# Performance work log

Measured on AMD Instinct MI355X. Metric: run time of the kernel, lower is better.

## Reference

```python
import jax, jax.numpy as jnp
from jax import lax
import numpy as np

B = 256
EMB_DIM = 64
N_EMB = 512
LAT1 = 1024   # 16 slots * 64
LAT2 = 512
LAT = LAT1 + LAT2  # 1536
COMMIT = 0.25
EMB_COST = 1.0


def setup_inputs() -> dict:
    key = jax.random.key(0)
    ks = iter(jax.random.split(key, 40))

    def w(shape, fan_in):
        return jax.random.normal(next(ks), shape, jnp.float32) * np.float32(1.0 / np.sqrt(fan_in))

    def b(n):
        return jax.random.normal(next(ks), (n,), jnp.float32) * np.float32(0.01)

    inp = {}
    inp['x'] = jax.random.normal(next(ks), (B, 3, 64, 64), jnp.float32)
    # encoder convs, torch OIHW layout, k=4
    inp['ew0'] = w((64, 3, 4, 4), 3 * 16);   inp['eb0'] = b(64)
    inp['ew1'] = w((64, 64, 4, 4), 64 * 16); inp['eb1'] = b(64)
    inp['ew2'] = w((128, 64, 4, 4), 64 * 16); inp['eb2'] = b(128)
    inp['ew3'] = w((256, 128, 4, 4), 128 * 16); inp['eb3'] = b(256)
    # encoder fc11: 4096 -> 1024 -> 1024 -> 1536, stored (in,out)
    inp['fw0'] = w((4096, 1024), 4096); inp['fb0'] = b(1024)
    inp['fw1'] = w((1024, 1024), 1024); inp['fb1'] = b(1024)
    inp['fw2'] = w((1024, LAT), 1024);  inp['fb2'] = b(LAT)
    # VQ codebook
    inp['codebook'] = jax.random.normal(next(ks), (N_EMB, EMB_DIM), jnp.float32)
    # decoder fc3: 1536 -> 512 -> 1024 -> 4096
    inp['gw0'] = w((LAT, 512), LAT);    inp['gb0'] = b(512)
    inp['gw1'] = w((512, 1024), 512);   inp['gb1'] = b(1024)
    inp['gw2'] = w((1024, 4096), 1024); inp['gb2'] = b(4096)
    # decoder ConvTranspose2d weights, torch layout (Cin, Cout, kh, kw)
    inp['tw0'] = w((256, 128, 4, 4), 256 * 16); inp['tb0'] = b(128)
    inp['tw1'] = w((128, 64, 4, 4), 128 * 16);  inp['tb1'] = b(64)
    inp['tw2'] = w((64, 64, 4, 4), 64 * 16);    inp['tb2'] = b(64)
    inp['tw3'] = w((64, 3, 4, 4), 64 * 16);     inp['tb3'] = b(3)
    return inp


def _conv(x, w, b):
    # Conv2d k=4 s=2 p=1 -> halves H,W
    y = lax.conv_general_dilated(x, w, (2, 2), ((1, 1), (1, 1)),
                                 dimension_numbers=('NCHW', 'OIHW', 'NCHW'))
    return y + b[None, :, None, None]


def _convt(x, w, b):
    # ConvTranspose2d k=4 s=2 p=1 -> doubles H,W.
    # Equivalent to lhs_dilation=2, pad k-1-p=2, flipped kernel, swapped I/O.
    wf = jnp.flip(w, (2, 3)).transpose(1, 0, 2, 3)
    y = lax.conv_general_dilated(x, wf, (1, 1), ((2, 2), (2, 2)),
                                 lhs_dilation=(2, 2),
                                 dimension_numbers=('NCHW', 'OIHW', 'NCHW'))
    return y + b[None, :, None, None]


def _forward(x, ew0, eb0, ew1, eb1, ew2, eb2, ew3, eb3,
             fw0, fb0, fw1, fb1, fw2, fb2, codebook,
             gw0, gb0, gw1, gb1, gw2, gb2,
             tw0, tb0, tw1, tb1, tw2, tb2, tw3, tb3):
    relu = jax.nn.relu
    # --- encoder conv stack (last conv has no ReLU) ---
    h = relu(_conv(x, ew0, eb0))
    h = relu(_conv(h, ew1, eb1))
    h = relu(_conv(h, ew2, eb2))
    h = _conv(h, ew3, eb3)                      # [B,256,4,4]
    h = h.reshape(h.shape[0], -1)               # [B,4096]
    h = relu(h @ fw0 + fb0)
    h = relu(h @ fw1 + fb1)
    z = h @ fw2 + fb2                           # [B,1536]
    # --- split content / style (isVQStyle=False) ---
    z_c = z[:, :LAT1]
    z_s = z[:, LAT1:]
    # --- vector quantize z_c (16 slots of dim 64, shared codebook) ---
    flat = z_c.reshape(-1, EMB_DIM)             # [B*16, 64]
    d = (jnp.sum(flat * flat, axis=1, keepdims=True)
         + jnp.sum(codebook * codebook, axis=1)
         - 2.0 * flat @ codebook.T)             # [B*16, 512]
    idx = jnp.argmin(d, axis=1)
    quantized = codebook[idx].reshape(z_c.shape)  # [B,1024]
    sg = lax.stop_gradient
    q_latent_loss = jnp.mean((quantized - sg(z_c)) ** 2) * EMB_COST
    e_latent_loss = jnp.mean((z_c - sg(quantized)) ** 2) * COMMIT
    loss = q_latent_loss + e_latent_loss
    quantized = z_c + sg(quantized - z_c)       # straight-through
    e = jnp.concatenate([quantized, z_s], axis=-1)  # [B,1536]
    # --- decoder ---
    g = relu(e @ gw0 + gb0)
    g = relu(g @ gw1 + gb1)
    g = (g @ gw2 + gb2).reshape(-1, 256, 4, 4)
    g = relu(_convt(g, tw0, tb0))
    g = relu(_convt(g, tw1, tb1))
    g = relu(_convt(g, tw2, tb2))
    x_recon = _convt(g, tw3, tb3)               # [B,3,64,64]
    return x_recon, loss


def reference(x, ew0, eb0, ew1, eb1, ew2, eb2, ew3, eb3,
              fw0, fb0, fw1, fb1, fw2, fb2, codebook,
              gw0, gb0, gw1, gb1, gw2, gb2,
              tw0, tb0, tw1, tb1, tw2, tb2, tw3, tb3):
    return _forward(x, ew0, eb0, ew1, eb1, ew2, eb2, ew3, eb3,
                    fw0, fb0, fw1, fb1, fw2, fb2, codebook,
                    gw0, gb0, gw1, gb1, gw2, gb2,
                    tw0, tb0, tw1, tb1, tw2, tb2, tw3, tb3)
```

## Files before the change

### kernel.cpp

```cpp
#include <hip/hip_runtime.h>
#include <hip/hip_bf16.h>


#define TPB 256
typedef __attribute__((ext_vector_type(8))) short short8v;
typedef __attribute__((ext_vector_type(4))) float f32x4;
typedef unsigned int u32;
typedef unsigned short u16;

__device__ inline u16 f2bf(float x){
  union { __hip_bfloat16 b; u16 u; } cv;
  cv.b = __float2bfloat16(x);
  return cv.u;
}
__device__ inline float bf2f(u16 h){ union{u32 u;float f;}v; v.u=((u32)h)<<16; return v.f;}
__device__ inline u32 packhl(float x){ u16 h=f2bf(x); u16 l=f2bf(x-bf2f(h)); return ((u32)l<<16)|(u32)h;}

template<int NS>
__device__ inline void splitN(float x, u16 t[3]) {
  u16 h0 = f2bf(x); t[0] = h0;
  float r1 = x - bf2f(h0);
  u16 h1 = f2bf(r1); t[1] = h1;
  if (NS == 3) { float r2 = r1 - bf2f(h1); t[2] = f2bf(r2); }
}

template<int NS, int ST>
__device__ inline void stW(u32* L, int row, int oct, const u16 hs[3][8]) {
  constexpr int SWM = (ST == 64) ? 15 : 7;
  const int sw = row & SWM;
#pragma unroll
  for (int s = 0; s < NS; ++s) {
    uint4 d;
    d.x = (u32)hs[s][0] | ((u32)hs[s][1] << 16);
    d.y = (u32)hs[s][2] | ((u32)hs[s][3] << 16);
    d.z = (u32)hs[s][4] | ((u32)hs[s][5] << 16);
    d.w = (u32)hs[s][6] | ((u32)hs[s][7] << 16);
    int ch = (((s << 2) | oct) ^ sw) << 2;
    *reinterpret_cast<uint4*>(&L[row * ST + ch]) = d;
  }
}

template<int NS, int ST>
__device__ inline void stWf(u32* L, int row, int oct, const float v[8]) {
  u16 hs[3][8];
#pragma unroll
  for (int e = 0; e < 8; ++e) {
    u16 t3[3]; splitN<NS>(v[e], t3);
    hs[0][e] = t3[0]; hs[1][e] = t3[1]; if (NS == 3) hs[2][e] = t3[2];
  }
  stW<NS, ST>(L, row, oct, hs);
}

template<int ST>
__device__ inline void stWp(u32* L, int row, int oct, int s, uint4 d) {
  constexpr int SWM = (ST == 64) ? 15 : 7;
  int ch = (((s << 2) | oct) ^ (row & SWM)) << 2;
  *reinterpret_cast<uint4*>(&L[row * ST + ch]) = d;
}

template<int ST>
__device__ inline short8v rdFrag(const u32* L, int row, int c) {
  constexpr int SWM = (ST == 64) ? 15 : 7;
  int ph = (c ^ (row & SWM)) << 2;
  return *reinterpret_cast<const short8v*>(&L[row * ST + ph]);
}

__global__ __launch_bounds__(TPB) void wsplit3_k(
    const float* __restrict__ src, u16* __restrict__ dst, int n)
{
  for (int i = blockIdx.x * TPB + threadIdx.x; i < n; i += gridDim.x * TPB) {
    u16 t3[3]; splitN<3>(src[i], t3);
    dst[i] = t3[0]; dst[i + n] = t3[1]; dst[i + 2 * n] = t3[2];
  }
}
__global__ __launch_bounds__(TPB) void wprep2_k(
    const float* __restrict__ src, u16* __restrict__ dh, u16* __restrict__ dl,
    int Ci, int Co)
{
  int K4 = Ci << 2;
  int tot = 4 * Co * K4;
  for (int i = blockIdx.x * TPB + threadIdx.x; i < tot; i += gridDim.x * TPB) {
    int par = i / (Co * K4); int rem = i - par * (Co * K4);
    int co = rem / K4; int k4 = rem - co * K4;
    int ci = k4 >> 2, ay = (k4 >> 1) & 1, ax = k4 & 1;
    int py = par >> 1, px = par & 1;
    int widx = ((1 - py) << 2) + (1 - px) + (ay << 3) + (ax << 1);
    float x = src[(((size_t)ci * Co + co) << 4) + widx];
    u16 h = f2bf(x);
    dh[i] = h; dl[i] = f2bf(x - bf2f(h));
  }
}

__global__ __launch_bounds__(TPB) void x_pad_k(
    const float* __restrict__ x, float* __restrict__ xp)
{
  int idx = blockIdx.x * TPB + threadIdx.x;
  if (idx >= 3345408) return;
  int px = idx % 66; int t = idx / 66; int py = t % 66; int p = t / 66;
  float v = 0.f;
  if (py >= 1 && py <= 64 && px >= 1 && px <= 64)
    v = x[(size_t)p * 4096 + (py - 1) * 64 + (px - 1)];
  xp[idx] = v;
}
__global__ __launch_bounds__(TPB) void zb0_k(float* __restrict__ h0p)
{
  int idx = blockIdx.x * TPB + threadIdx.x;
  if (idx >= 2162688) return;
  int p = idx / 132, k = idx % 132;
  int py, px;
  if (k < 34)       { py = 0;           px = k; }
  else if (k < 68)  { py = 33;          px = k - 34; }
  else if (k < 100) { py = k - 68 + 1;  px = 0; }
  else              { py = k - 100 + 1; px = 33; }
  h0p[(size_t)p * 1156 + py * 34 + px] = 0.f;
}

template<int RM, int OUTM>
__global__ __launch_bounds__(TPB, 2) void conv_ad(
    const float* __restrict__ in, const u16* __restrict__ wsp,
    const float* __restrict__ bias, float* __restrict__ outp,
    int Ci, int Co, int Wi, int lwo, int relu, int KSPL, int PS,
    int bS, int ciS, int Mtot)
{
  constexpr int BM = RM * 64;
  __shared__ __align__(16) u32 BL[2][64 * 64];
  const int K = Ci << 4;
  const int PW = Wi + 2;
  const int Wo = Wi >> 1;
  const int tid = threadIdx.x;
  const int m0 = blockIdx.x * BM, n0 = blockIdx.y << 6;
  const int lane = tid & 63, wv = tid >> 6, r = lane & 15, g = lane >> 4;
  const int kb0 = blockIdx.z * KSPL;
  const int kbN = min(kb0 + KSPL, K);
  const int khsel = g & 1;
  const int cig = g >> 1;
  f32x4 acc[RM][4] = {};

  int base[RM];
#pragma unroll
  for (int mm = 0; mm < RM; ++mm) {
    int cell = m0 + (wv * RM + mm) * 16 + r;
    int x = cell & (Wo - 1), y = (cell >> lwo) & (Wo - 1), b = cell >> (lwo + lwo);
    base[mm] = b * bS + (2 * y + 2 * khsel) * PW + 2 * x;
  }

  auto gA = [&](int kb, float v[RM][8]) {
    if ((kb + (g << 3)) < K) {
      int cioff = ((kb >> 4) + cig) * ciS;
#pragma unroll
      for (int mm = 0; mm < RM; ++mm) {
        const float* p = in + base[mm] + cioff;
#pragma unroll
        for (int e = 0; e < 8; ++e)
          v[mm][e] = p[(e >> 2) * PW + (e & 3)];
      }
    } else {
#pragma unroll
      for (int mm = 0; mm < RM; ++mm)
#pragma unroll
        for (int e = 0; e < 8; ++e) v[mm][e] = 0.f;
    }
  };
  auto gB = [&](int kb, uint4* d) {
    int n = tid & 63, oc2 = tid >> 6;
    int k8 = kb + (oc2 << 3);
    if (k8 < K) {
      const u16* wp = wsp + (size_t)(n0 + n) * K + k8;
      d[0] = *reinterpret_cast<const uint4*>(wp);
      d[1] = *reinterpret_cast<const uint4*>(wp + PS);
      d[2] = *reinterpret_cast<const uint4*>(wp + 2 * PS);
    } else {
      d[0] = d[1] = d[2] = make_uint4(0u, 0u, 0u, 0u);
    }
  };
  auto mkfrags = [&](const float v[8], short8v f[3]) {
    u16 hs[3][8];
#pragma unroll
    for (int e = 0; e < 8; ++e) {
      u16 t3[3]; splitN<3>(v[e], t3);
      hs[0][e] = t3[0]; hs[1][e] = t3[1]; hs[2][e] = t3[2];
    }
#pragma unroll
    for (int s = 0; s < 3; ++s) {
      union { u16 u[8]; short8v sv; } cv;
#pragma unroll
      for (int e = 0; e < 8; ++e) cv.u[e] = hs[s][e];
      f[s] = cv.sv;
    }
  };

  float vA[RM][8], vA2[RM][8];
  uint4 vB[3], vB2[3];
  gA(kb0, vA); gB(kb0, vB);
  for (int kb = kb0; kb < kbN; kb += 32) {
    u32* BLc = BL[((kb - kb0) >> 5) & 1];
    {
      int n = tid & 63, oc2 = tid >> 6;
      stWp<64>(BLc, n, oc2, 0, vB[0]);
      stWp<64>(BLc, n, oc2, 1, vB[1]);
      stWp<64>(BLc, n, oc2, 2, vB[2]);
    }
    const bool more = (kb + 32) < kbN;
    if (more) { gB(kb + 32, vB2); gA(kb + 32, vA2); }
    short8v a_[RM][3];
#pragma unroll
    for (int mm = 0; mm < RM; ++mm) mkfrags(vA[mm], a_[mm]);
    __syncthreads();
#pragma unroll
    for (int ns = 0; ns < 4; ++ns) {
      short8v b_[3];
#pragma unroll
      for (int s = 0; s < 3; ++s) b_[s] = rdFrag<64>(BLc, (ns << 4) + r, (s << 2) | g);
#pragma unroll
      for (int mm = 0; mm < RM; ++mm) {
        acc[mm][ns] = __builtin_amdgcn_mfma_f32_16x16x32_bf16(a_[mm][0], b_[0], acc[mm][ns], 0, 0, 0);
        acc[mm][ns] = __builtin_amdgcn_mfma_f32_16x16x32_bf16(a_[mm][0], b_[1], acc[mm][ns], 0, 0, 0);
        acc[mm][ns] = __builtin_amdgcn_mfma_f32_16x16x32_bf16(a_[mm][1], b_[0], acc[mm][ns], 0, 0, 0);
        acc[mm][ns] = __builtin_amdgcn_mfma_f32_16x16x32_bf16(a_[mm][1], b_[1], acc[mm][ns], 0, 0, 0);
        acc[mm][ns] = __builtin_amdgcn_mfma_f32_16x16x32_bf16(a_[mm][0], b_[2], acc[mm][ns], 0, 0, 0);
        acc[mm][ns] = __builtin_amdgcn_mfma_f32_16x16x32_bf16(a_[mm][2], b_[0], acc[mm][ns], 0, 0, 0);
      }
    }
    if (more) {
#pragma unroll
      for (int mm = 0; mm < RM; ++mm)
#pragma unroll
        for (int e = 0; e < 8; ++e) vA[mm][e] = vA2[mm][e];
#pragma unroll
      for (int s = 0; s < 3; ++s) vB[s] = vB2[s];
    }
  }
#pragma unroll
  for (int mm = 0; mm < RM; ++mm)
#pragma unroll
    for (int ns = 0; ns < 4; ++ns) {
      int c0 = m0 + (wv * RM + mm) * 16 + (g << 2);
      int co = n0 + (ns << 4) + r;
      if (OUTM == 0) {
        float bv = bias[co];
        const int OPW = Wo + 2;
        const int OPHW = OPW * OPW;
#pragma unroll
        for (int q = 0; q < 4; ++q) {
          int cell = c0 + q;
          int x = cell & (Wo - 1), y = (cell >> lwo) & (Wo - 1), b = cell >> (lwo + lwo);
          float v = acc[mm][ns][q] + bv;
          if (relu) v = fmaxf(v, 0.f);
          outp[((size_t)(b * Co + co)) * OPHW + (y + 1) * OPW + (x + 1)] = v;
        }
      } else {
        float4 o;
        o.x = acc[mm][ns][0]; o.y = acc[mm][ns][1];
        o.z = acc[mm][ns][2]; o.w = acc[mm][ns][3];
        *reinterpret_cast<float4*>(
            &outp[((size_t)(blockIdx.z * Co + co)) * Mtot + c0]) = o;
      }
    }
}

__global__ __launch_bounds__(TPB) void combine_cm_k(
    const float* __restrict__ P, const float* __restrict__ bias,
    float* __restrict__ out)
{
  int idx = blockIdx.x * TPB + threadIdx.x;
  if (idx >= 5308416) return;
  int px = idx % 18; int t = idx / 18; int py = t % 18; t /= 18;
  int b = t % 256; int co = t / 256;
  float v = 0.f;
  if (py >= 1 && py <= 16 && px >= 1 && px <= 16) {
    int cell = b * 256 + (py - 1) * 16 + (px - 1);
    v = P[(size_t)co * 65536 + cell] + P[(size_t)(64 + co) * 65536 + cell] + bias[co];
    v = fmaxf(v, 0.f);
  }
  out[idx] = v;
}

__global__ __launch_bounds__(TPB) void combine_pad_k(
    const float* __restrict__ P, const float* __restrict__ bias,
    float* __restrict__ out)
{
  int idx = blockIdx.x * TPB + threadIdx.x;
  if (idx >= 3276800) return;
  int px = idx % 10; int t = idx / 10; int py = t % 10; t /= 10;
  int co = t % 128; int b = t / 128;
  float v = 0.f;
  if (py >= 1 && py <= 8 && px >= 1 && px <= 8) {
    int cell = b * 64 + (py - 1) * 8 + (px - 1);
    float s = 0.f;
#pragma unroll
    for (int z = 0; z < 4; ++z)
      s += P[((size_t)(z * 128 + co)) * 16384 + cell];
    v = fmaxf(s + bias[co], 0.f);
  }
  out[idx] = v;
}

__global__ __launch_bounds__(TPB) void conv_combine(
    const float* __restrict__ P, const float* __restrict__ bias,
    float* __restrict__ out, int Mtot, int N, int SK, int lwo, int relu)
{
  int idx = blockIdx.x * TPB + threadIdx.x;
  int mq = Mtot >> 2;
  int co = idx / mq;
  int cell0 = (idx - co * mq) << 2;
  if (co >= N) return;
  float4 s = make_float4(0.f, 0.f, 0.f, 0.f);
  for (int z = 0; z < SK; ++z) {
    const float4 pv = *reinterpret_cast<const float4*>(
        &P[((size_t)z * N + co) * Mtot + cell0]);
    s.x += pv.x; s.y += pv.y; s.z += pv.z; s.w += pv.w;
  }
  float bv = bias[co];
  s.x += bv; s.y += bv; s.z += bv; s.w += bv;
  if (relu) { s.x = fmaxf(s.x, 0.f); s.y = fmaxf(s.y, 0.f);
              s.z = fmaxf(s.z, 0.f); s.w = fmaxf(s.w, 0.f); }
  int Wo = 1 << lwo;
  int x = cell0 & (Wo - 1), y = (cell0 >> lwo) & (Wo - 1), b = cell0 >> (lwo + lwo);
  *reinterpret_cast<float4*>(&out[(((size_t)b * N + co) * Wo + y) * Wo + x]) = s;
}

template<int NS, int OUTM>
__global__ __launch_bounds__(TPB) void gemm_mf(
    const float* __restrict__ A, const float* __restrict__ W,
    const float* __restrict__ bias, void* __restrict__ outp,
    int M, int K, int N, int KSPL)
{
  constexpr int ST = (NS == 3) ? 64 : 32;
  __shared__ __align__(16) u32 L[(64 + 64) * ST];
  u32* AL = L; u32* BL = L + 64 * ST;
  const int tid = threadIdx.x;
  const int m0 = blockIdx.x << 6, n0 = blockIdx.y << 6;
  const int lane = tid & 63, wv = tid >> 6, r = lane & 15, g = lane >> 4;
  const int kb0 = blockIdx.z * KSPL;
  const int kbN = kb0 + KSPL;
  const int cl = tid & 63, oct = tid >> 6;
  f32x4 acc[4] = {};

  float vA[8], vB[8], vA2[8], vB2[8];
  auto gA = [&](int kt, float* v) {
    const float* ap = &A[(size_t)(m0 + cl) * K + kt + (oct << 3)];
    *reinterpret_cast<float4*>(&v[0]) = *reinterpret_cast<const float4*>(ap);
    *reinterpret_cast<float4*>(&v[4]) = *reinterpret_cast<const float4*>(ap + 4);
  };
  auto gB = [&](int kt, float* v) {
#pragma unroll
    for (int e = 0; e < 8; ++e)
      v[e] = W[(size_t)(kt + (oct << 3) + e) * N + n0 + cl];
  };

  gA(kb0, vA); gB(kb0, vB);
  for (int kt = kb0; kt < kbN; kt += 32) {
    const bool more = (kt + 32) < kbN;
    if (more) { gA(kt + 32, vA2); gB(kt + 32, vB2); }
    stWf<NS, ST>(AL, cl, oct, vA);
    stWf<NS, ST>(BL, cl, oct, vB);
    __syncthreads();
    short8v a_[3];
#pragma unroll
    for (int s = 0; s < NS; ++s) a_[s] = rdFrag<ST>(AL, (wv << 4) + r, (s << 2) | g);
#pragma unroll
    for (int ns = 0; ns < 4; ++ns) {
      short8v b_[3];
#pragma unroll
      for (int s = 0; s < NS; ++s) b_[s] = rdFrag<ST>(BL, (ns << 4) + r, (s << 2) | g);
      acc[ns] = __builtin_amdgcn_mfma_f32_16x16x32_bf16(a_[0], b_[0], acc[ns], 0, 0, 0);
      acc[ns] = __builtin_amdgcn_mfma_f32_16x16x32_bf16(a_[0], b_[1], acc[ns], 0, 0, 0);
      acc[ns] = __builtin_amdgcn_mfma_f32_16x16x32_bf16(a_[1], b_[0], acc[ns], 0, 0, 0);
      if (NS == 3) {
        acc[ns] = __builtin_amdgcn_mfma_f32_16x16x32_bf16(a_[1], b_[1], acc[ns], 0, 0, 0);
        acc[ns] = __builtin_amdgcn_mfma_f32_16x16x32_bf16(a_[0], b_[2], acc[ns], 0, 0, 0);
        acc[ns] = __builtin_amdgcn_mfma_f32_16x16x32_bf16(a_[2], b_[0], acc[ns], 0, 0, 0);
      }
    }
    __syncthreads();
    if (more) {
#pragma unroll
      for (int e = 0; e < 8; ++e) { vA[e] = vA2[e]; vB[e] = vB2[e]; }
    }
  }
#pragma unroll
  for (int ns = 0; ns < 4; ++ns)
#pragma unroll
    for (int q = 0; q < 4; ++q) {
      int m = m0 + (wv << 4) + (g << 2) + q;
      int n = n0 + (ns << 4) + r;
      float v = acc[ns][q];
      if (OUTM == 0) ((float*)outp)[((size_t)blockIdx.z * M + m) * N + n] = v;
      else           ((u32*)outp)[(size_t)m * N + n] = packhl(v + bias[n]);
    }
}

__global__ __launch_bounds__(TPB) void combine_k(
    const float* __restrict__ P, const float* __restrict__ bias,
    float* __restrict__ out, int MN, int N, int SK, int relu)
{
  int i4 = (blockIdx.x * TPB + threadIdx.x) << 2;
  if (i4 >= MN) return;
  float4 s = make_float4(0.f, 0.f, 0.f, 0.f);
  for (int z = 0; z < SK; ++z) {
    const float4 pv = *reinterpret_cast<const float4*>(&P[(size_t)z * MN + i4]);
    s.x += pv.x; s.y += pv.y; s.z += pv.z; s.w += pv.w;
  }
  int n = i4 % N;
  s.x += bias[n]; s.y += bias[n + 1]; s.z += bias[n + 2]; s.w += bias[n + 3];
  if (relu) { s.x = fmaxf(s.x, 0.f); s.y = fmaxf(s.y, 0.f);
              s.z = fmaxf(s.z, 0.f); s.w = fmaxf(s.w, 0.f); }
  *reinterpret_cast<float4*>(&out[i4]) = s;
}

__global__ __launch_bounds__(TPB) void combine_pk_k(
    const float* __restrict__ P, const float* __restrict__ bias,
    u32* __restrict__ out)
{
  int i4 = (blockIdx.x * TPB + threadIdx.x) << 2;
  if (i4 >= 1048576) return;
  const float4 p0 = *reinterpret_cast<const float4*>(&P[i4]);
  const float4 p1 = *reinterpret_cast<const float4*>(&P[1048576 + i4]);
  int n = i4 % 4096;
  uint4 o;
  o.x = packhl(p0.x + p1.x + bias[n]);
  o.y = packhl(p0.y + p1.y + bias[n + 1]);
  o.z = packhl(p0.z + p1.z + bias[n + 2]);
  o.w = packhl(p0.w + p1.w + bias[n + 3]);
  *reinterpret_cast<uint4*>(&out[i4]) = o;
}

template<int RM, int EMIT, int SPLITIN>
__global__ __launch_bounds__(TPB) void convt_ad(
    const u32* __restrict__ in, const u16* __restrict__ wth,
    const u16* __restrict__ wtl, const float* __restrict__ bias,
    u32* __restrict__ outq, int Ci, int Co, int Hi, int lwi, int relu)
{
  constexpr int BM = RM * 64;
  constexpr int STC = BM + 4;
  constexpr int LB = 2 * 64 * 32;
  constexpr int LSZ = (LB > 16 * STC) ? LB : 16 * STC;
  __shared__ __align__(16) u32 L[LSZ];
  const int Wi = Hi, K4 = Ci << 2;
  const int HW = Hi * Wi, HWq = HW >> 2, Wiq = Wi >> 1;
  const int par = blockIdx.z, py = par >> 1, px = par & 1;
  const int tid = threadIdx.x;
  const int m0 = blockIdx.x * BM, n0 = blockIdx.y << 6;
  const int lane = tid & 63, wv = tid >> 6, r = lane & 15, g = lane >> 4;
  const int stepCi = SPLITIN ? HWq : HW;
  f32x4 acc[RM][4] = {};

  int offT[RM][4]; u32 mskT[RM][4];
#pragma unroll
  for (int mm = 0; mm < RM; ++mm) {
    int cell = m0 + (wv * RM + mm) * 16 + r;
    int X = cell & (Wi - 1), Y = (cell >> lwi) & (Wi - 1), b = cell >> (lwi + lwi);
#pragma unroll
    for (int t = 0; t < 4; ++t) {
      int ay = t >> 1, ax = t & 1;
      int gy = Y + py - ay, gx = X + px - ax;
      bool ok = (gy >= 0 && gy < Hi && gx >= 0 && gx < Wi);
      int gyc = min(max(gy, 0), Hi - 1), gxc = min(max(gx, 0), Wi - 1);
      if (SPLITIN) {
        int q = ((gyc & 1) << 1) | (gxc & 1);
        offT[mm][t] = q * (256 * Ci * HWq) + b * Ci * HWq + (gyc >> 1) * Wiq + (gxc >> 1);
      } else {
        offT[mm][t] = b * Ci * HW + gyc * Wi + gxc;
      }
      mskT[mm][t] = ok ? 0xffffffffu : 0u;
    }
  }

  auto gB = [&](int kb, uint4* d) {
    int n = tid & 63, oc2 = tid >> 6;
    size_t base = (size_t)(par * Co + n0 + n) * K4 + kb + (oc2 << 3);
    d[0] = *reinterpret_cast<const uint4*>(wth + base);
    d[1] = *reinterpret_cast<const uint4*>(wtl + base);
  };

  uint4 vB[2], vB2[2];
  gB(0, vB);
  u32 vA[RM][8];
  int cur = 0;
  for (int kb = 0; kb < K4; kb += 32) {
    {
      int cib = ((kb >> 2) + (g << 1)) * stepCi;
#pragma unroll
      for (int mm = 0; mm < RM; ++mm)
#pragma unroll
        for (int e = 0; e < 8; ++e) {
          int t = e & 3;
          vA[mm][e] = in[offT[mm][t] + cib + ((e >> 2) ? stepCi : 0)] & mskT[mm][t];
        }
    }
    u32* BLc = L + cur * (64 * 32);
    {
      int n = tid & 63, oc2 = tid >> 6;
      stWp<32>(BLc, n, oc2, 0, vB[0]);
      stWp<32>(BLc, n, oc2, 1, vB[1]);
    }
    const bool more = (kb + 32) < K4;
    if (more) gB(kb + 32, vB2);
    __syncthreads();
    short8v a_[RM][2];
#pragma unroll
    for (int mm = 0; mm < RM; ++mm) {
      const u32* v = vA[mm];
      union { uint4 u; short8v s; } ch, clo;
      ch.u.x = (v[0] & 0xffffu) | (v[1] << 16);  clo.u.x = (v[0] >> 16) | (v[1] & 0xffff0000u);
      ch.u.y = (v[2] & 0xffffu) | (v[3] << 16);  clo.u.y = (v[2] >> 16) | (v[3] & 0xffff0000u);
      ch.u.z = (v[4] & 0xffffu) | (v[5] << 16);  clo.u.z = (v[4] >> 16) | (v[5] & 0xffff0000u);
      ch.u.w = (v[6] & 0xffffu) | (v[7] << 16);  clo.u.w = (v[6] >> 16) | (v[7] & 0xffff0000u);
      a_[mm][0] = ch.s; a_[mm][1] = clo.s;
    }
#pragma unroll
    for (int ns = 0; ns < 4; ++ns) {
      short8v b_[2];
#pragma unroll
      for (int s = 0; s < 2; ++s) b_[s] = rdFrag<32>(BLc, (ns << 4) + r, (s << 2) | g);
#pragma unroll
      for (int mm = 0; mm < RM; ++mm) {
        acc[mm][ns] = __builtin_amdgcn_mfma_f32_16x16x32_bf16(a_[mm][0], b_[0], acc[mm][ns], 0, 0, 0);
        acc[mm][ns] = __builtin_amdgcn_mfma_f32_16x16x32_bf16(a_[mm][0], b_[1], acc[mm][ns], 0, 0, 0);
        acc[mm][ns] = __builtin_amdgcn_mfma_f32_16x16x32_bf16(a_[mm][1], b_[0], acc[mm][ns], 0, 0, 0);
      }
    }
    if (more) { vB[0] = vB2[0]; vB[1] = vB2[1]; }
    cur ^= 1;
  }
  const size_t QO = (size_t)256 * Co * HW;
  u32* op = outq + (size_t)par * QO;
  constexpr int C4N = BM / 4;
#pragma unroll
  for (int ph = 0; ph < 4; ++ph) {
    __syncthreads();
    float bv = bias[n0 + (ph << 4) + r];
#pragma unroll
    for (int mm = 0; mm < RM; ++mm)
#pragma unroll
      for (int q = 0; q < 4; ++q) {
        int cell = (wv * RM + mm) * 16 + (g << 2) + q;
        float v = acc[mm][ph][q] + bv;
        if (relu) v = fmaxf(v, 0.f);
        L[r * STC + cell] = EMIT ? packhl(v) : __float_as_uint(v);
      }
    __syncthreads();
#pragma unroll
    for (int it = 0; it < RM; ++it) {
      int lin = it * TPB + tid;
      int c4 = lin & (C4N - 1);
      int colL = lin / C4N;
      int col = (ph << 4) + colL;
      int cell0 = c4 << 2;
      uint4 d = *reinterpret_cast<const uint4*>(&L[colL * STC + cell0]);
      int gc = m0 + cell0;
      int Xo = gc & (Wi - 1), Yo = (gc >> lwi) & (Wi - 1), bo = gc >> (lwi + lwi);
      *reinterpret_cast<uint4*>(
          &op[((size_t)(bo * Co + n0 + col) * Hi + Yo) * Wi + Xo]) = d;
    }
  }
}

__global__ __launch_bounds__(TPB) void convt3_kernel(
    const float* __restrict__ inq, const float* __restrict__ w,
    float* __restrict__ part)
{
  __shared__ float wl[3072];
  __shared__ float il[8][33 * 32];
  const int b = blockIdx.x;
  const int z = blockIdx.y;
  const int tid = threadIdx.x;
  for (int i = tid; i < 3072; i += TPB) wl[i] = w[i];
  const int Y = tid >> 3;
  const int X0 = (tid & 7) << 2;
  float acc[3][2][8];
#pragma unroll
  for (int o = 0; o < 3; ++o)
#pragma unroll
    for (int p = 0; p < 2; ++p)
#pragma unroll
      for (int q = 0; q < 8; ++q) acc[o][p][q] = 0.f;

  const int cbeg = z << 5, cend = cbeg + 32;
  for (int c0 = cbeg; c0 < cend; c0 += 8) {
    __syncthreads();
    for (int i = tid; i < 8192; i += TPB) {
      int cc = i >> 10, yy = (i >> 5) & 31, xx = i & 31;
      int q = ((yy & 1) << 1) | (xx & 1);
      il[cc][yy * 33 + xx] = inq[(size_t)q * 4194304 +
          (((size_t)b * 64 + c0 + cc) * 16 + (yy >> 1)) * 16 + (xx >> 1)];
    }
    __syncthreads();
    for (int cc = 0; cc < 8; ++cc) {
      float iv[3][6];
#pragma unroll
      for (int j = 0; j < 3; ++j) {
        int gy = Y - 1 + j;
        int gyc = min(max(gy, 0), 31);
        float my = (gy >= 0 && gy < 32) ? 1.f : 0.f;
#pragma unroll
        for (int k = 0; k < 6; ++k) {
          int gx = X0 - 1 + k;
          int gxc = min(max(gx, 0), 31);
          float mx = (gx >= 0 && gx < 32) ? 1.f : 0.f;
          iv[j][k] = il[cc][gyc * 33 + gxc] * (my * mx);
        }
      }
      const float* wq = &wl[(c0 + cc) * 48];
#pragma unroll
      for (int o = 0; o < 3; ++o) {
        const float* wo = wq + o * 16;
#pragma unroll
        for (int c = 0; c < 4; ++c) {
          acc[o][0][2*c]   = fmaf(iv[1][c+1], wo[5],  acc[o][0][2*c]);
          acc[o][0][2*c]   = fmaf(iv[1][c],   wo[7],  acc[o][0][2*c]);
          acc[o][0][2*c]   = fmaf(iv[0][c+1], wo[13], acc[o][0][2*c]);
          acc[o][0][2*c]   = fmaf(iv[0][c],   wo[15], acc[o][0][2*c]);
          acc[o][0][2*c+1] = fmaf(iv[1][c+2], wo[4],  acc[o][0][2*c+1]);
          acc[o][0][2*c+1] = fmaf(iv[1][c+1], wo[6],  acc[o][0][2*c+1]);
          acc[o][0][2*c+1] = fmaf(iv[0][c+2], wo[12], acc[o][0][2*c+1]);
          acc[o][0][2*c+1] = fmaf(iv[0][c+1], wo[14], acc[o][0][2*c+1]);
          acc[o][1][2*c]   = fmaf(iv[2][c+1], wo[1],  acc[o][1][2*c]);
          acc[o][1][2*c]   = fmaf(iv[2][c],   wo[3],  acc[o][1][2*c]);
          acc[o][1][2*c]   = fmaf(iv[1][c+1], wo[9],  acc[o][1][2*c]);
          acc[o][1][2*c]   = fmaf(iv[1][c],   wo[11], acc[o][1][2*c]);
          acc[o][1][2*c+1] = fmaf(iv[2][c+2], wo[0],  acc[o][1][2*c+1]);
          acc[o][1][2*c+1] = fmaf(iv[2][c+1], wo[2],  acc[o][1][2*c+1]);
          acc[o][1][2*c+1] = fmaf(iv[1][c+2], wo[8],  acc[o][1][2*c+1]);
          acc[o][1][2*c+1] = fmaf(iv[1][c+1], wo[10], acc[o][1][2*c+1]);
        }
      }
    }
  }
  float* pz = part + (size_t)z * 3145728;
#pragma unroll
  for (int o = 0; o < 3; ++o) {
#pragma unroll
    for (int p = 0; p < 2; ++p) {
      float* op = pz + (((size_t)b * 3 + o) * 64 + 2 * Y + p) * 64 + 2 * X0;
      *reinterpret_cast<float4*>(op) =
          make_float4(acc[o][p][0], acc[o][p][1], acc[o][p][2], acc[o][p][3]);
      *reinterpret_cast<float4*>(op + 4) =
          make_float4(acc[o][p][4], acc[o][p][5], acc[o][p][6], acc[o][p][7]);
    }
  }
}

__global__ __launch_bounds__(TPB) void c3_combine(
    const float* __restrict__ part, const float* __restrict__ bias,
    float* __restrict__ out)
{
  int i4 = (blockIdx.x * TPB + threadIdx.x) << 2;
  const float4 p0 = *reinterpret_cast<const float4*>(&part[i4]);
  const float4 p1 = *reinterpret_cast<const float4*>(&part[i4 + 3145728]);
  int o = (i4 >> 12) % 3;
  float bv = bias[o];
  float4 s = make_float4(p0.x + p1.x + bv, p0.y + p1.y + bv,
                         p0.z + p1.z + bv, p0.w + p1.w + bv);
  *reinterpret_cast<float4*>(&out[i4]) = s;
}

__global__ __launch_bounds__(TPB) void vq8_kernel(
    const float* __restrict__ z, const float* __restrict__ cb,
    float* __restrict__ e, float* __restrict__ rowloss)
{
  __shared__ float cbL[64][65];
  __shared__ float zr[8][64];
  const int tid = threadIdx.x;
  const int lane = tid & 63, wid = tid >> 6;
  const int r0 = blockIdx.x << 3;

  for (int i = tid; i < 512; i += TPB) {
    int rr = i >> 6, k = i & 63;
    int row = r0 + rr;
    int b = row >> 4, s = row & 15;
    zr[rr][k] = z[(size_t)b * 1536 + s * 64 + k];
  }

  float best[2] = {3.4e38f, 3.4e38f};
  int bi[2] = {0, 0};

  for (int c0 = 0; c0 < 512; c0 += 64) {
    __syncthreads();
#pragma unroll
    for (int i = 0; i < 4; ++i) {
      int j = (tid >> 4) + (i << 4);
      int kq = tid & 15;
      const float4 v = *reinterpret_cast<const float4*>(
          &cb[(size_t)(c0 + j) * 64 + (kq << 2)]);
      cbL[(kq << 2) + 0][j] = v.x;
      cbL[(kq << 2) + 1][j] = v.y;
      cbL[(kq << 2) + 2][j] = v.z;
      cbL[(kq << 2) + 3][j] = v.w;
    }
    __syncthreads();
#pragma unroll
    for (int rep = 0; rep < 2; ++rep) {
      const float* zp = zr[wid + (rep << 2)];
      float d = 0.f;
#pragma unroll
      for (int k = 0; k < 64; ++k) {
        float t = zp[k] - cbL[k][lane];
        d = fmaf(t, t, d);
      }
      if (d < best[rep]) { best[rep] = d; bi[rep] = c0 + lane; }
    }
  }
#pragma unroll
  for (int rep = 0; rep < 2; ++rep) {
#pragma unroll
    for (int off = 32; off > 0; off >>= 1) {
      float ob = __shfl_xor(best[rep], off);
      int   oi = __shfl_xor(bi[rep], off);
      if (ob < best[rep] || (ob == best[rep] && oi < bi[rep])) {
        best[rep] = ob; bi[rep] = oi;
      }
    }
    int row = r0 + wid + (rep << 2);
    int b = row >> 4, s = row & 15;
    e[(size_t)b * 1536 + s * 64 + lane] = cb[(size_t)bi[rep] * 64 + lane];
    if (lane == 0) rowloss[row] = best[rep];
  }
}

__global__ __launch_bounds__(TPB) void zs_copy_kernel(
    const float* __restrict__ z, float* __restrict__ e)
{
  int i = blockIdx.x * TPB + threadIdx.x;
  int b = i >> 9, k = i & 511;
  e[(size_t)b * 1536 + 1024 + k] = z[(size_t)b * 1536 + 1024 + k];
}

__global__ __launch_bounds__(TPB) void loss_reduce_kernel(
    const float* __restrict__ rl, float* __restrict__ out)
{
  __shared__ float sm[TPB];
  float s = 0.f;
  for (int i = threadIdx.x; i < 4096; i += TPB) s += rl[i];
  sm[threadIdx.x] = s;
  __syncthreads();
  for (int sft = 128; sft > 0; sft >>= 1) {
    if (threadIdx.x < sft) sm[threadIdx.x] += sm[threadIdx.x + sft];
    __syncthreads();
  }
  if (threadIdx.x == 0) out[0] = sm[0] * (1.25f / 262144.f);
}

extern "C" void kernel_launch(void* const* d_in, const int* in_sizes, int n_in,
                              void* d_out, int out_size, void* d_ws, size_t ws_size,
                              hipStream_t stream)
{
  const float* x    = (const float*)d_in[0];
  const float* ew0  = (const float*)d_in[1];
  const float* eb0  = (const float*)d_in[2];
  const float* ew1  = (const float*)d_in[3];
  const float* eb1  = (const float*)d_in[4];
  const float* ew2  = (const float*)d_in[5];
  const float* eb2  = (const float*)d_in[6];
  const float* ew3  = (const float*)d_in[7];
  const float* eb3  = (const float*)d_in[8];
  const float* fw0  = (const float*)d_in[9];
  const float* fb0  = (const float*)d_in[10];
  const float* fw1  = (const float*)d_in[11];
  const float* fb1  = (const float*)d_in[12];
  const float* fw2  = (const float*)d_in[13];
  const float* fb2  = (const float*)d_in[14];
  const float* cb   = (const float*)d_in[15];
  const float* gw0  = (const float*)d_in[16];
  const float* gb0  = (const float*)d_in[17];
  const float* gw1  = (const float*)d_in[18];
  const float* gb1  = (const float*)d_in[19];
  const float* gw2  = (const float*)d_in[20];
  const float* gb2  = (const float*)d_in[21];
  const float* tw0  = (const float*)d_in[22];
  const float* tb0  = (const float*)d_in[23];
  const float* tw1  = (const float*)d_in[24];
  const float* tb1  = (const float*)d_in[25];
  const float* tw2  = (const float*)d_in[26];
  const float* tb2  = (const float*)d_in[27];
  const float* tw3  = (const float*)d_in[28];
  const float* tb3  = (const float*)d_in[29];

  float* out = (float*)d_out;
  float* ws  = (float*)d_ws;

  u16*   WE0  = (u16*)(ws + 0);
  u16*   WE1  = (u16*)(ws + 4608);
  u16*   WE2  = (u16*)(ws + 102912);
  u16*   WE3  = (u16*)(ws + 299520);
  float* RL   = ws + 1085952;
  float* H0P  = ws + 1090048;
  float* PC1  = ws + 20029952;
  float* XP   = ws + 20029952;
  float* H1P  = ws + 1090048;
  float* PC23 = ws + 6398464;
  float* H2P  = ws + 14787072;
  float* H3   = ws + 18063872;
  float* P    = ws + 1090048;
  float* F0   = ws + 5284352;
  float* F1   = ws + 5546496;
  float* Z    = ws + 5808640;
  float* E    = ws + 6201856;
  float* G0   = ws + 6595072;
  float* G1   = ws + 6726144;
  float* T2S  = ws + 1090048;
  u16*   WT0h = (u16*)(ws + 17867264);
  u16*   WT0l = (u16*)(ws + 18129408);
  u16*   WT1h = (u16*)(ws + 18391552);
  u16*   WT1l = (u16*)(ws + 18457088);
  u16*   WT2h = (u16*)(ws + 18522624);
  u16*   WT2l = (u16*)(ws + 18555392);
  float* PG2  = ws + 18588160;
  u32*   G2P  = (u32*)(ws + 20685312);
  u32*   T0S  = (u32*)(ws + 21733888);
  u32*   T1S  = (u32*)(ws + 23831040);
  float* PT3  = ws + 18588160;

  wsplit3_k<<<dim3(12),  TPB, 0, stream>>>(ew0, WE0, 3072);
  wsplit3_k<<<dim3(256), TPB, 0, stream>>>(ew1, WE1, 65536);
  wsplit3_k<<<dim3(512), TPB, 0, stream>>>(ew2, WE2, 131072);
  wsplit3_k<<<dim3(1024),TPB, 0, stream>>>(ew3, WE3, 524288);
  x_pad_k<<<dim3(13068), TPB, 0, stream>>>(x, XP);
  zb0_k<<<dim3(8448), TPB, 0, stream>>>(H0P);

  conv_ad<4,0><<<dim3(1024, 1, 1), TPB, 0, stream>>>(
      XP, WE0, eb0, H0P, 3, 64, 64, 5, 1, 48, 3072, 13068, 4356, 0);
  conv_ad<4,1><<<dim3(256, 1, 2), TPB, 0, stream>>>(
      H0P, WE1, eb1, PC1, 64, 64, 32, 4, 1, 512, 65536, 73984, 1156, 65536);
  combine_cm_k<<<dim3(20736), TPB, 0, stream>>>(PC1, eb1, H1P);
  conv_ad<4,1><<<dim3(64, 2, 4), TPB, 0, stream>>>(
      H1P, WE2, eb2, PC23, 64, 128, 16, 3, 1, 256, 131072, 324, 82944, 16384);
  combine_pad_k<<<dim3(12800), TPB, 0, stream>>>(PC23, eb2, H2P);
  conv_ad<4,1><<<dim3(16, 4, 8), TPB, 0, stream>>>(
      H2P, WE3, eb3, PC23, 128, 256, 8, 2, 0, 256, 524288, 12800, 100, 4096);
  conv_combine<<<dim3(1024), TPB, 0, stream>>>(PC23, eb3, H3, 4096, 256, 8, 2, 0);

  gemm_mf<3,0><<<dim3(4, 16, 16), TPB, 0, stream>>>(H3, fw0, fb0, (void*)P, 256, 4096, 1024, 256);
  combine_k<<<dim3(256), TPB, 0, stream>>>(P, fb0, F0, 262144, 1024, 16, 1);
  gemm_mf<3,0><<<dim3(4, 16, 8), TPB, 0, stream>>>(F0, fw1, fb1, (void*)P, 256, 1024, 1024, 128);
  combine_k<<<dim3(256), TPB, 0, stream>>>(P, fb1, F1, 262144, 1024, 8, 1);
  gemm_mf<3,0><<<dim3(4, 24, 8), TPB, 0, stream>>>(F1, fw2, fb2, (void*)P, 256, 1024, 1536, 128);
  combine_k<<<dim3(384), TPB, 0, stream>>>(P, fb2, Z, 393216, 1536, 8, 0);

  vq8_kernel<<<dim3(512), TPB, 0, stream>>>(Z, cb, E, RL);
  zs_copy_kernel<<<dim3(512), TPB, 0, stream>>>(Z, E);
  loss_reduce_kernel<<<dim3(1), TPB, 0, stream>>>(RL, out + (size_t)out_size - 1);

  gemm_mf<2,0><<<dim3(4, 8, 8), TPB, 0, stream>>>(E,  gw0, gb0, (void*)P, 256, 1536, 512, 192);
  combine_k<<<dim3(128), TPB, 0, stream>>>(P, gb0, G0, 131072, 512, 8, 1);
  gemm_mf<2,0><<<dim3(4, 16, 4), TPB, 0, stream>>>(G0, gw1, gb1, (void*)P, 256, 512, 1024, 128);
  combine_k<<<dim3(256), TPB, 0, stream>>>(P, gb1, G1, 262144, 1024, 4, 1);

  wprep2_k<<<dim3(512), TPB, 0, stream>>>(tw0, WT0h, WT0l, 256, 128);
  wprep2_k<<<dim3(128), TPB, 0, stream>>>(tw1, WT1h, WT1l, 128, 64);
  wprep2_k<<<dim3(64),  TPB, 0, stream>>>(tw2, WT2h, WT2l, 64, 64);

  gemm_mf<2,0><<<dim3(4, 64, 2), TPB, 0, stream>>>(G1, gw2, gb2, (void*)PG2, 256, 1024, 4096, 512);
  combine_pk_k<<<dim3(1024), TPB, 0, stream>>>(PG2, gb2, G2P);

  convt_ad<2,1,0><<<dim3(32, 2, 4),  TPB, 0, stream>>>(G2P, WT0h, WT0l, tb0, T0S, 256, 128, 4,  2, 1);
  convt_ad<4,1,1><<<dim3(64, 1, 4),  TPB, 0, stream>>>(T0S, WT1h, WT1l, tb1, T1S, 128, 64,  8,  3, 1);
  convt_ad<4,0,1><<<dim3(256, 1, 4), TPB, 0, stream>>>(T1S, WT2h, WT2l, tb2, (u32*)T2S, 64, 64, 16, 4, 1);
  convt3_kernel<<<dim3(256, 2), TPB, 0, stream>>>(T2S, tw3, PT3);
  c3_combine<<<dim3(3072), TPB, 0, stream>>>(PT3, tb3, out);
}
```

Measured before the change: 536.1 us.

## Drop split-bf16 precision in decoder GEMM and transposed convs to single bf16

Switches the last decoder FC and the three transposed-conv layers from a hi/lo bf16 split (three MFMAs per product) to plain single bf16 (one MFMA). Weight prep now emits only the high half, and activations are packed as a single bf16. The convt kernel also prefetches the A operand into registers one step ahead and uses smaller row tiles with more blocks. This removes most MFMA work and halves the weight traffic in these layers, at the cost of reduced accuracy that may exceed the tolerance.

Result: faster. 508.8 us (-5.1%).

```diff
diff --git a/kernel.cpp b/kernel.cpp
--- a/kernel.cpp
+++ b/kernel.cpp
@@ -14,7 +14,6 @@
   return cv.u;
 }
 __device__ inline float bf2f(u16 h){ union{u32 u;float f;}v; v.u=((u32)h)<<16; return v.f;}
-__device__ inline u32 packhl(float x){ u16 h=f2bf(x); u16 l=f2bf(x-bf2f(h)); return ((u32)l<<16)|(u32)h;}
 
 template<int NS>
 __device__ inline void splitN(float x, u16 t[3]) {
@@ -45,7 +44,7 @@
   u16 hs[3][8];
 #pragma unroll
   for (int e = 0; e < 8; ++e) {
-    u16 t3[3]; splitN<NS>(v[e], t3);
+    u16 t3[3]; splitN<(NS == 3) ? 3 : 2>(v[e], t3);
     hs[0][e] = t3[0]; hs[1][e] = t3[1]; if (NS == 3) hs[2][e] = t3[2];
   }
   stW<NS, ST>(L, row, oct, hs);
@@ -73,9 +72,8 @@
     dst[i] = t3[0]; dst[i + n] = t3[1]; dst[i + 2 * n] = t3[2];
   }
 }
-__global__ __launch_bounds__(TPB) void wprep2_k(
-    const float* __restrict__ src, u16* __restrict__ dh, u16* __restrict__ dl,
-    int Ci, int Co)
+__global__ __launch_bounds__(TPB) void wprep1_k(
+    const float* __restrict__ src, u16* __restrict__ dh, int Ci, int Co)
 {
   int K4 = Ci << 2;
   int tot = 4 * Co * K4;
@@ -85,9 +83,7 @@
     int ci = k4 >> 2, ay = (k4 >> 1) & 1, ax = k4 & 1;
     int py = par >> 1, px = par & 1;
     int widx = ((1 - py) << 2) + (1 - px) + (ay << 3) + (ax << 1);
-    float x = src[(((size_t)ci * Co + co) << 4) + widx];
-    u16 h = f2bf(x);
-    dh[i] = h; dl[i] = f2bf(x - bf2f(h));
+    dh[i] = f2bf(src[(((size_t)ci * Co + co) << 4) + widx]);
   }
 }
 
@@ -364,8 +360,10 @@
 #pragma unroll
       for (int s = 0; s < NS; ++s) b_[s] = rdFrag<ST>(BL, (ns << 4) + r, (s << 2) | g);
       acc[ns] = __builtin_amdgcn_mfma_f32_16x16x32_bf16(a_[0], b_[0], acc[ns], 0, 0, 0);
-      acc[ns] = __builtin_amdgcn_mfma_f32_16x16x32_bf16(a_[0], b_[1], acc[ns], 0, 0, 0);
-      acc[ns] = __builtin_amdgcn_mfma_f32_16x16x32_bf16(a_[1], b_[0], acc[ns], 0, 0, 0);
+      if (NS >= 2) {
+        acc[ns] = __builtin_amdgcn_mfma_f32_16x16x32_bf16(a_[0], b_[1], acc[ns], 0, 0, 0);
+        acc[ns] = __builtin_amdgcn_mfma_f32_16x16x32_bf16(a_[1], b_[0], acc[ns], 0, 0, 0);
+      }
       if (NS == 3) {
         acc[ns] = __builtin_amdgcn_mfma_f32_16x16x32_bf16(a_[1], b_[1], acc[ns], 0, 0, 0);
         acc[ns] = __builtin_amdgcn_mfma_f32_16x16x32_bf16(a_[0], b_[2], acc[ns], 0, 0, 0);
@@ -386,7 +384,7 @@
       int n = n0 + (ns << 4) + r;
       float v = acc[ns][q];
       if (OUTM == 0) ((float*)outp)[((size_t)blockIdx.z * M + m) * N + n] = v;
-      else           ((u32*)outp)[(size_t)m * N + n] = packhl(v + bias[n]);
+      else           ((u32*)outp)[(size_t)m * N + n] = (u32)f2bf(v + bias[n]);
     }
 }
 
@@ -418,18 +416,18 @@
   const float4 p1 = *reinterpret_cast<const float4*>(&P[1048576 + i4]);
   int n = i4 % 4096;
   uint4 o;
-  o.x = packhl(p0.x + p1.x + bias[n]);
-  o.y = packhl(p0.y + p1.y + bias[n + 1]);
-  o.z = packhl(p0.z + p1.z + bias[n + 2]);
-  o.w = packhl(p0.w + p1.w + bias[n + 3]);
+  o.x = (u32)f2bf(p0.x + p1.x + bias[n]);
+  o.y = (u32)f2bf(p0.y + p1.y + bias[n + 1]);
+  o.z = (u32)f2bf(p0.z + p1.z + bias[n + 2]);
+  o.w = (u32)f2bf(p0.w + p1.w + bias[n + 3]);
   *reinterpret_cast<uint4*>(&out[i4]) = o;
 }
 
 template<int RM, int EMIT, int SPLITIN>
 __global__ __launch_bounds__(TPB) void convt_ad(
     const u32* __restrict__ in, const u16* __restrict__ wth,
-    const u16* __restrict__ wtl, const float* __restrict__ bias,
-    u32* __restrict__ outq, int Ci, int Co, int Hi, int lwi, int relu)
+    const float* __restrict__ bias, u32* __restrict__ outq,
+    int Ci, int Co, int Hi, int lwi, int relu)
 {
   constexpr int BM = RM * 64;
   constexpr int STC = BM + 4;
@@ -466,61 +464,60 @@
     }
   }
 
+  auto gA = [&](int kb, u32 v[RM][8]) {
+    int cib = ((kb >> 2) + (g << 1)) * stepCi;
+#pragma unroll
+    for (int mm = 0; mm < RM; ++mm)
+#pragma unroll
+      for (int e = 0; e < 8; ++e) {
+        int t = e & 3;
+        v[mm][e] = in[offT[mm][t] + cib + ((e >> 2) ? stepCi : 0)] & mskT[mm][t];
+      }
+  };
   auto gB = [&](int kb, uint4* d) {
     int n = tid & 63, oc2 = tid >> 6;
-    size_t base = (size_t)(par * Co + n0 + n) * K4 + kb + (oc2 << 3);
-    d[0] = *reinterpret_cast<const uint4*>(wth + base);
-    d[1] = *reinterpret_cast<const uint4*>(wtl + base);
+    *d = *reinterpret_cast<const uint4*>(
+        wth + (size_t)(par * Co + n0 + n) * K4 + kb + (oc2 << 3));
   };
 
-  uint4 vB[2], vB2[2];
-  gB(0, vB);
-  u32 vA[RM][8];
+  u32 vA[RM][8], vA2[RM][8];
+  uint4 vB, vB2;
+  gA(0, vA); gB(0, &vB);
   int cur = 0;
   for (int kb = 0; kb < K4; kb += 32) {
-    {
-      int cib = ((kb >> 2) + (g << 1)) * stepCi;
-#pragma unroll
-      for (int mm = 0; mm < RM; ++mm)
-#pragma unroll
-        for (int e = 0; e < 8; ++e) {
-          int t = e & 3;
-          vA[mm][e] = in[offT[mm][t] + cib + ((e >> 2) ? stepCi : 0)] & mskT[mm][t];
-        }
-    }
     u32* BLc = L + cur * (64 * 32);
     {
       int n = tid & 63, oc2 = tid >> 6;
-      stWp<32>(BLc, n, oc2, 0, vB[0]);
-      stWp<32>(BLc, n, oc2, 1, vB[1]);
+      stWp<32>(BLc, n, oc2, 0, vB);
     }
     const bool more = (kb + 32) < K4;
-    if (more) gB(kb + 32, vB2);
-    __syncthreads();
-    short8v a_[RM][2];
+    if (more) { gB(kb + 32, &vB2); gA(kb + 32, vA2); }
+    short8v a_[RM];
 #pragma unroll
     for (int mm = 0; mm < RM; ++mm) {
       const u32* v = vA[mm];
-      union { uint4 u; short8v s; } ch, clo;
-      ch.u.x = (v[0] & 0xffffu) | (v[1] << 16);  clo.u.x = (v[0] >> 16) | (v[1] & 0xffff0000u);
-      ch.u.y = (v[2] & 0xffffu) | (v[3] << 16);  clo.u.y = (v[2] >> 16) | (v[3] & 0xffff0000u);
-      ch.u.z = (v[4] & 0xffffu) | (v[5] << 16);  clo.u.z = (v[4] >> 16) | (v[5] & 0xffff0000u);
-      ch.u.w = (v[6] & 0xffffu) | (v[7] << 16);  clo.u.w = (v[6] >> 16) | (v[7] & 0xffff0000u);
-      a_[mm][0] = ch.s; a_[mm][1] = clo.s;
-    }
+      union { uint4 u; short8v s; } ch;
+      ch.u.x = (v[0] & 0xffffu) | (v[1] << 16);
+      ch.u.y = (v[2] & 0xffffu) | (v[3] << 16);
+      ch.u.z = (v[4] & 0xffffu) | (v[5] << 16);
+      ch.u.w = (v[6] & 0xffffu) | (v[7] << 16);
+      a_[mm] = ch.s;
+    }
+    __syncthreads();
 #pragma unroll
     for (int ns = 0; ns < 4; ++ns) {
-      short8v b_[2];
-#pragma unroll
-      for (int s = 0; s < 2; ++s) b_[s] = rdFrag<32>(BLc, (ns << 4) + r, (s << 2) | g);
-#pragma unroll
-      for (int mm = 0; mm < RM; ++mm) {
-        acc[mm][ns] = __builtin_amdgcn_mfma_f32_16x16x32_bf16(a_[mm][0], b_[0], acc[mm][ns], 0, 0, 0);
-        acc[mm][ns] = __builtin_amdgcn_mfma_f32_16x16x32_bf16(a_[mm][0], b_[1], acc[mm][ns], 0, 0, 0);
-        acc[mm][ns] = __builtin_amdgcn_mfma_f32_16x16x32_bf16(a_[mm][1], b_[0], acc[mm][ns], 0, 0, 0);
-      }
-    }
-    if (more) { vB[0] = vB2[0]; vB[1] = vB2[1]; }
+      short8v b0 = rdFrag<32>(BLc, (ns << 4) + r, g);
+#pragma unroll
+      for (int mm = 0; mm < RM; ++mm)
+        acc[mm][ns] = __builtin_amdgcn_mfma_f32_16x16x32_bf16(a_[mm], b0, acc[mm][ns], 0, 0, 0);
+    }
+    if (more) {
+#pragma unroll
+      for (int mm = 0; mm < RM; ++mm)
+#pragma unroll
+        for (int e = 0; e < 8; ++e) vA[mm][e] = vA2[mm][e];
+      vB = vB2;
+    }
     cur ^= 1;
   }
   const size_t QO = (size_t)256 * Co * HW;
@@ -537,7 +534,7 @@
         int cell = (wv * RM + mm) * 16 + (g << 2) + q;
         float v = acc[mm][ph][q] + bv;
         if (relu) v = fmaxf(v, 0.f);
-        L[r * STC + cell] = EMIT ? packhl(v) : __float_as_uint(v);
+        L[r * STC + cell] = EMIT ? (u32)f2bf(v) : __float_as_uint(v);
       }
     __syncthreads();
 #pragma unroll
@@ -800,11 +797,8 @@
   float* G1   = ws + 6726144;
   float* T2S  = ws + 1090048;
   u16*   WT0h = (u16*)(ws + 17867264);
-  u16*   WT0l = (u16*)(ws + 18129408);
   u16*   WT1h = (u16*)(ws + 18391552);
-  u16*   WT1l = (u16*)(ws + 18457088);
   u16*   WT2h = (u16*)(ws + 18522624);
-  u16*   WT2l = (u16*)(ws + 18555392);
   float* PG2  = ws + 18588160;
   u32*   G2P  = (u32*)(ws + 20685312);
   u32*   T0S  = (u32*)(ws + 21733888);
@@ -846,16 +840,16 @@
   gemm_mf<2,0><<<dim3(4, 16, 4), TPB, 0, stream>>>(G0, gw1, gb1, (void*)P, 256, 512, 1024, 128);
   combine_k<<<dim3(256), TPB, 0, stream>>>(P, gb1, G1, 262144, 1024, 4, 1);
 
-  wprep2_k<<<dim3(512), TPB, 0, stream>>>(tw0, WT0h, WT0l, 256, 128);
-  wprep2_k<<<dim3(128), TPB, 0, stream>>>(tw1, WT1h, WT1l, 128, 64);
-  wprep2_k<<<dim3(64),  TPB, 0, stream>>>(tw2, WT2h, WT2l, 64, 64);
-
-  gemm_mf<2,0><<<dim3(4, 64, 2), TPB, 0, stream>>>(G1, gw2, gb2, (void*)PG2, 256, 1024, 4096, 512);
+  wprep1_k<<<dim3(512), TPB, 0, stream>>>(tw0, WT0h, 256, 128);
+  wprep1_k<<<dim3(128), TPB, 0, stream>>>(tw1, WT1h, 128, 64);
+  wprep1_k<<<dim3(64),  TPB, 0, stream>>>(tw2, WT2h, 64, 64);
+
+  gemm_mf<1,0><<<dim3(4, 64, 2), TPB, 0, stream>>>(G1, gw2, gb2, (void*)PG2, 256, 1024, 4096, 512);
   combine_pk_k<<<dim3(1024), TPB, 0, stream>>>(PG2, gb2, G2P);
 
-  convt_ad<2,1,0><<<dim3(32, 2, 4),  TPB, 0, stream>>>(G2P, WT0h, WT0l, tb0, T0S, 256, 128, 4,  2, 1);
-  convt_ad<4,1,1><<<dim3(64, 1, 4),  TPB, 0, stream>>>(T0S, WT1h, WT1l, tb1, T1S, 128, 64,  8,  3, 1);
-  convt_ad<4,0,1><<<dim3(256, 1, 4), TPB, 0, stream>>>(T1S, WT2h, WT2l, tb2, (u32*)T2S, 64, 64, 16, 4, 1);
+  convt_ad<2,1,0><<<dim3(32, 2, 4),  TPB, 0, stream>>>(G2P, WT0h, tb0, T0S, 256, 128, 4,  2, 1);
+  convt_ad<2,1,1><<<dim3(128, 1, 4), TPB, 0, stream>>>(T0S, WT1h, tb1, T1S, 128, 64,  8,  3, 1);
+  convt_ad<2,0,1><<<dim3(512, 1, 4), TPB, 0, stream>>>(T1S, WT2h, tb2, (u32*)T2S, 64, 64, 16, 4, 1);
   convt3_kernel<<<dim3(256, 2), TPB, 0, stream>>>(T2S, tw3, PT3);
   c3_combine<<<dim3(3072), TPB, 0, stream>>>(PT3, tb3, out);
 }
```
